# Kernel optimization log

Hardware: AMD Instinct MI355X
Metric: run time of the kernel (lower is better)

The kernel has to match this reference:

```python
import jax, jax.numpy as jnp
import numpy as np

B, S, D, H, L = 32, 1024, 512, 8, 4
DH = D // H
FF = D            # dim_feedforward == hidden_dim in the original ctor call
LOC_D, TD_D = 16, 8
TD_EMB = 3        # time_dist_embed_dim
POI = 21          # poi vocab
POI_EMB = 3
ADDR_IN = 1 + POI_EMB
FC = 32           # fc_hidden_dim
NEG = -1e9


def setup_inputs() -> dict:
    key = jax.random.key(0)
    ks = jax.random.split(key, 20)
    g = lambda i, shape, s=0.02: jax.random.normal(ks[i], shape, jnp.float32) * s
    return {
        "addr": jax.random.normal(ks[0], (B, 1), jnp.float32),
        "loc_dense_seq": jax.random.normal(ks[1], (B, S, LOC_D), jnp.float32),
        "time_dist_seq": jax.random.normal(ks[2], (B, S, TD_D), jnp.float32),
        "Wtd": g(3, (TD_D, TD_EMB)), "btd": jnp.zeros((TD_EMB,), jnp.float32),
        "Wemb": g(4, (LOC_D + TD_EMB, D)), "bemb": jnp.zeros((D,), jnp.float32),
        "Wqkv": g(5, (L, D, 3 * D)), "bqkv": jnp.zeros((L, 3 * D), jnp.float32),
        "Wo": g(6, (L, D, D)), "bo": jnp.zeros((L, D), jnp.float32),
        "ln1_g": jnp.ones((L, D), jnp.float32), "ln1_b": jnp.zeros((L, D), jnp.float32),
        "W1": g(7, (L, D, FF)), "b1": jnp.zeros((L, FF), jnp.float32),
        "W2": g(8, (L, FF, D)), "b2": jnp.zeros((L, D), jnp.float32),
        "ln2_g": jnp.ones((L, D), jnp.float32), "ln2_b": jnp.zeros((L, D), jnp.float32),
        "poi_emb": g(9, (POI, POI_EMB), 1.0),
        "Wa": g(10, (ADDR_IN, FC)), "ba": jnp.zeros((FC,), jnp.float32),
        "Wout": g(11, (D, FC)),
        "Wcomb": g(12, (FC, 1)),
        "addr_type": jax.random.randint(ks[13], (B, 1), 0, POI),
        "data_length": jax.random.randint(ks[14], (B,), 1, S + 1),
    }


def _ln(x, g, b, eps=1e-5):
    m = x.mean(-1, keepdims=True)
    v = ((x - m) ** 2).mean(-1, keepdims=True)
    return (x - m) / jnp.sqrt(v + eps) * g + b


def reference(addr, loc_dense_seq, time_dist_seq, Wtd, btd, Wemb, bemb, Wqkv,
              bqkv, Wo, bo, ln1_g, ln1_b, W1, b1, W2, b2, ln2_g, ln2_b,
              poi_emb, Wa, ba, Wout, Wcomb, addr_type, data_length):
    valid = jnp.arange(S)[None, :] < data_length[:, None]            # [B,S]
    td = time_dist_seq @ Wtd + btd                                   # [B,S,3]
    x = jnp.concatenate([loc_dense_seq, td], axis=-1) @ Wemb + bemb  # [B,S,D]
    scale = 1.0 / jnp.sqrt(jnp.float32(DH))
    for l in range(L):  # post-norm TransformerEncoderLayer (relu, eval/no-dropout)
        qkv = x @ Wqkv[l] + bqkv[l]
        q, k, v = jnp.split(qkv, 3, axis=-1)
        q = q.reshape(B, S, H, DH)
        k = k.reshape(B, S, H, DH)
        v = v.reshape(B, S, H, DH)
        scores = jnp.einsum('bqhd,bkhd->bhqk', q, k) * scale
        scores = jnp.where(valid[:, None, None, :], scores, NEG)     # mask padded keys
        attn = jax.nn.softmax(scores, axis=-1)
        ctx = jnp.einsum('bhqk,bkhd->bqhd', attn, v).reshape(B, S, D)
        x = _ln(x + ctx @ Wo[l] + bo[l], ln1_g[l], ln1_b[l])
        ff = jax.nn.relu(x @ W1[l] + b1[l]) @ W2[l] + b2[l]
        x = _ln(x + ff, ln2_g[l], ln2_b[l])
    # per-sample addr branch (vectorized over the original python loop)
    addr_inp = jnp.concatenate([addr, poi_emb[addr_type[:, 0]]], axis=-1)  # [B,4]
    a = addr_inp @ Wa + ba                                                 # [B,FC]
    o = (jnp.tanh(x @ Wout + a[:, None, :]) @ Wcomb)[..., 0]              # [B,S]
    logits = jnp.where(valid, o, NEG)
    logp = jax.nn.log_softmax(logits, axis=1)  # log_softmax over valid positions only
    return jnp.where(valid, logp, 0.0)
```

## Files before the change

kernel.cpp:

```cpp
#include <hip/hip_runtime.h>
#include <stdint.h>


typedef unsigned short u16;
typedef __attribute__((ext_vector_type(8))) short short8;
typedef __attribute__((ext_vector_type(4))) float f32x4;

constexpr int Bn = 32, Sn = 1024, Dn = 512, Ln = 4;
constexpr int BS = Bn * Sn;
constexpr size_t QKV_OFF = 16777216;

__device__ __forceinline__ float b2f(u16 u) {
    union { uint32_t i; float f; } v; v.i = ((uint32_t)u) << 16; return v.f;
}
__device__ __forceinline__ u16 f2b(float f) {
    union { float f; uint32_t i; } v; v.f = f;
    uint32_t r = v.i + 0x7fffu + ((v.i >> 16) & 1u);
    return (u16)(r >> 16);
}
__device__ __forceinline__ float getf(const void* p, size_t i, int F) {
    return F ? ((const float*)p)[i] : b2f(((const u16*)p)[i]);
}
__device__ __forceinline__ void cp16(void* lds, const void* g) {
    __builtin_amdgcn_global_load_lds(
        (__attribute__((address_space(1))) void*)(uintptr_t)g,
        (__attribute__((address_space(3))) void*)(uint32_t)(uintptr_t)lds,
        16, 0, 0);
}
__device__ __forceinline__ float asf(uint32_t u) {
    union { uint32_t i; float f; } v; v.i = u; return v.f;
}

__global__ __launch_bounds__(256)
void detect_kernel(const void* loc, int* flag)
{
    __shared__ int cnt;
    if (threadIdx.x == 0) cnt = 0;
    __syncthreads();
    const u16* p = (const u16*)loc;
    int c = 0;
    for (int i = threadIdx.x; i < 2048; i += 256) {
        const float v = b2f(p[i]);
        if (!(fabsf(v) <= 100.0f)) c++;
    }
    atomicAdd(&cnt, c);
    __syncthreads();
    if (threadIdx.x == 0) *flag = (cnt >= 64) ? 1 : 0;
}

__global__ __launch_bounds__(256)
void gemm_bt(const u16* __restrict__ A, const u16* __restrict__ Bt,
             const void* __restrict__ bias, int boff, u16* __restrict__ C,
             int N, int K, int relu, int mode, const int* __restrict__ flagp,
             const int* __restrict__ dlen)
{
    __shared__ __align__(16) u16 As[128 * 32];
    __shared__ __align__(16) u16 Bs[128 * 32];
    const int bn0 = blockIdx.x * 128, bm0 = blockIdx.y * 128;
    if ((bm0 & 1023) >= dlen[bm0 >> 10]) return;
    const int F = *flagp;
    const int tid = threadIdx.x;
    const int lane = tid & 63, w = tid >> 6;
    const int wm = w >> 1, wn = w & 1;
    const int quad = lane >> 4, l16 = lane & 15;

    const f32x4 vzero = {0.f, 0.f, 0.f, 0.f};
    f32x4 acc[4][4];
#pragma unroll
    for (int i = 0; i < 4; i++)
#pragma unroll
        for (int j = 0; j < 4; j++) acc[i][j] = vzero;

    const int i0 = tid, i1 = tid + 256;
    const u16* a0 = A + (size_t)(bm0 + (i0 >> 2)) * K + (i0 & 3) * 8;
    const u16* a1 = A + (size_t)(bm0 + (i1 >> 2)) * K + (i1 & 3) * 8;
    const u16* b0 = Bt + (size_t)(bn0 + (i0 >> 2)) * K + (i0 & 3) * 8;
    const u16* b1 = Bt + (size_t)(bn0 + (i1 >> 2)) * K + (i1 & 3) * 8;

    for (int k0 = 0; k0 < K; k0 += 32) {
        cp16(As + i0 * 8, a0 + k0);
        cp16(As + i1 * 8, a1 + k0);
        cp16(Bs + i0 * 8, b0 + k0);
        cp16(Bs + i1 * 8, b1 + k0);
        __syncthreads();
        short8 af[4], bfr[4];
#pragma unroll
        for (int t = 0; t < 4; t++)
            af[t] = *(const short8*)&As[(wm * 64 + t * 16 + l16) * 32 + quad * 8];
#pragma unroll
        for (int t = 0; t < 4; t++)
            bfr[t] = *(const short8*)&Bs[(wn * 64 + t * 16 + l16) * 32 + quad * 8];
#pragma unroll
        for (int tm = 0; tm < 4; tm++)
#pragma unroll
            for (int tn = 0; tn < 4; tn++)
                acc[tm][tn] = __builtin_amdgcn_mfma_f32_16x16x32_bf16(
                    af[tm], bfr[tn], acc[tm][tn], 0, 0, 0);
        __syncthreads();
    }
    const int bb = bm0 >> 10;
#pragma unroll
    for (int tm = 0; tm < 4; tm++)
#pragma unroll
        for (int tn = 0; tn < 4; tn++) {
            const int col = bn0 + wn * 64 + tn * 16 + l16;
            const float bv = getf(bias, (size_t)boff + col, F);
            if (mode == 0) {
#pragma unroll
                for (int r = 0; r < 4; r++) {
                    const int row = bm0 + wm * 64 + tm * 16 + quad * 4 + r;
                    float v = acc[tm][tn][r] + bv;
                    if (relu) v = fmaxf(v, 0.0f);
                    C[(size_t)row * N + col] = f2b(v);
                }
            } else {
                const int which = col >> 9;
                const int c = col & 511;
                const int hh = c >> 6, f = c & 63;
                u16* dst = C + (size_t)which * QKV_OFF
                           + (((size_t)(bb * 8 + hh)) << 16) + f;
#pragma unroll
                for (int r = 0; r < 4; r++) {
                    const int s = (bm0 & 1023) + wm * 64 + tm * 16 + quad * 4 + r;
                    dst[(size_t)s * 64] = f2b(acc[tm][tn][r] + bv);
                }
            }
        }
}

__global__ __launch_bounds__(256)
void attn_kernel(const u16* __restrict__ qp, const int* __restrict__ dlen,
                 u16* __restrict__ ctx)
{
    const int id = blockIdx.x;
    const int qt = 7 - (id >> 8);
    const int bh = id & 255;
    const int h = bh & 7, b = bh >> 3;
    const int len = dlen[b];
    if (qt * 128 >= len) return;
    const int tid = threadIdx.x, lane = tid & 63, w = tid >> 6;
    const int quad = lane >> 4, l16 = lane & 15;
    __shared__ __align__(16) u16 Vt[2][64 * 72];
    __shared__ __align__(16) u16 Pl[4][32 * 72];
    u16* Plw = Pl[w];
    const int sw = l16 & 3;
    const u16* qb = qp + ((size_t)bh << 16);
    const u16* kb = qb + QKV_OFF;
    const u16* vb = qb + 2 * QKV_OFF;
    const int q0 = qt * 128 + w * 32;
    constexpr float SC = 0.18033688011112043f;

    short8 qf[2][2];
#pragma unroll
    for (int sub = 0; sub < 2; sub++)
#pragma unroll
        for (int s = 0; s < 2; s++)
            qf[sub][s] = *(const short8*)(qb + (size_t)(q0 + sub * 16 + l16) * 64
                                          + quad * 8 + 32 * s);

    const int key2 = (tid & 31) * 2, f0 = (tid >> 5) * 8;
    const u16* vsrc = vb + f0;
    short8 v0 = *(const short8*)(vsrc + (size_t)key2 * 64);
    short8 v1 = *(const short8*)(vsrc + (size_t)(key2 + 1) * 64);

    short8 ones;
#pragma unroll
    for (int j = 0; j < 8; j++) ones[j] = (short)0x3F80;

    const f32x4 vzero = {0.f, 0.f, 0.f, 0.f};
    f32x4 O[2][4], lacc[2];
#pragma unroll
    for (int sub = 0; sub < 2; sub++) {
        lacc[sub] = vzero;
#pragma unroll
        for (int t = 0; t < 4; t++) O[sub][t] = vzero;
    }

    const int nkt = (len + 63) >> 6;
    int buf = 0;
    for (int kt = 0; kt < nkt; kt++) {
        const int k0 = kt * 64;
        u16* Vb = Vt[buf];
#pragma unroll
        for (int j = 0; j < 8; j++)
            *(uint32_t*)&Vb[(f0 + j) * 72 + key2] =
                (uint32_t)(u16)v0[j] | ((uint32_t)(u16)v1[j] << 16);
        __syncthreads();
        if (kt + 1 < nkt) {
            const u16* nv = vsrc + (size_t)(k0 + 64 + key2) * 64;
            v0 = *(const short8*)nv;
            v1 = *(const short8*)(nv + 64);
        }
        short8 kf[4][2];
#pragma unroll
        for (int tn = 0; tn < 4; tn++) {
            const u16* kp2 = kb + (size_t)(k0 + tn * 16 + l16) * 64 + quad * 8;
            kf[tn][0] = *(const short8*)kp2;
            kf[tn][1] = *(const short8*)(kp2 + 32);
        }
        const bool full = (k0 + 64 <= len);
#pragma unroll
        for (int sub = 0; sub < 2; sub++) {
            f32x4 sacc[4];
#pragma unroll
            for (int tn = 0; tn < 4; tn++) {
                f32x4 z = vzero;
                z = __builtin_amdgcn_mfma_f32_16x16x32_bf16(kf[tn][0], qf[sub][0], z, 0, 0, 0);
                sacc[tn] = __builtin_amdgcn_mfma_f32_16x16x32_bf16(kf[tn][1], qf[sub][1], z, 0, 0, 0);
            }
            const int prow = (sub * 16 + l16) * 72;
#pragma unroll
            for (int tn = 0; tn < 4; tn++) {
                float p[4];
                if (full) {
#pragma unroll
                    for (int r = 0; r < 4; r++) p[r] = exp2f(sacc[tn][r] * SC);
                } else {
                    const int kbnd = k0 + tn * 16 + quad * 4;
#pragma unroll
                    for (int r = 0; r < 4; r++)
                        p[r] = (kbnd + r < len) ? exp2f(sacc[tn][r] * SC) : 0.0f;
                }
                uint2 pk;
                pk.x = (__float_as_uint(p[0]) >> 16) | (__float_as_uint(p[1]) & 0xFFFF0000u);
                pk.y = (__float_as_uint(p[2]) >> 16) | (__float_as_uint(p[3]) & 0xFFFF0000u);
                *(uint2*)&Plw[prow + (((tn ^ sw) << 4) + quad * 4)] = pk;
            }
        }
        __builtin_amdgcn_wave_barrier();
#pragma unroll
        for (int s = 0; s < 2; s++) {
            const int tnr = ((quad >> 1) + 2 * s) ^ sw;
            short8 pf0 = *(const short8*)&Plw[(l16) * 72 + (tnr << 4) + (quad & 1) * 8];
            short8 pf1 = *(const short8*)&Plw[(16 + l16) * 72 + (tnr << 4) + (quad & 1) * 8];
            lacc[0] = __builtin_amdgcn_mfma_f32_16x16x32_bf16(pf0, ones, lacc[0], 0, 0, 0);
            lacc[1] = __builtin_amdgcn_mfma_f32_16x16x32_bf16(pf1, ones, lacc[1], 0, 0, 0);
#pragma unroll
            for (int t = 0; t < 4; t++) {
                short8 vf = *(const short8*)&Vb[(t * 16 + l16) * 72 + quad * 8 + 32 * s];
                O[0][t] = __builtin_amdgcn_mfma_f32_16x16x32_bf16(pf0, vf, O[0][t], 0, 0, 0);
                O[1][t] = __builtin_amdgcn_mfma_f32_16x16x32_bf16(pf1, vf, O[1][t], 0, 0, 0);
            }
        }
        __builtin_amdgcn_wave_barrier();
        buf ^= 1;
    }
#pragma unroll
    for (int sub = 0; sub < 2; sub++)
#pragma unroll
        for (int r = 0; r < 4; r++) {
            const float inv = 1.0f / lacc[sub][r];
            const int q = q0 + sub * 16 + quad * 4 + r;
#pragma unroll
            for (int t = 0; t < 4; t++)
                ctx[(size_t)(b * Sn + q) * Dn + h * 64 + t * 16 + l16] =
                    f2b(O[sub][t][r] * inv);
        }
}

__global__ __launch_bounds__(256)
void ln_res(u16* __restrict__ x, const u16* __restrict__ t,
            const void* __restrict__ g, const void* __restrict__ bta, int off,
            const int* __restrict__ flagp, const int* __restrict__ dlen)
{
    const int w = threadIdx.x >> 6, lane = threadIdx.x & 63;
    const size_t row = (size_t)blockIdx.x * 4 + w;
    if ((int)(row & 1023) >= dlen[row >> 10]) return;
    const int F = *flagp;
    u16* xp = x + row * Dn;
    const u16* tp = t + row * Dn;
    const int c0 = lane * 8;
    short8 xv = *(const short8*)(xp + c0);
    short8 tv = *(const short8*)(tp + c0);
    float v[8]; float s = 0.f;
#pragma unroll
    for (int i = 0; i < 8; i++) {
        v[i] = b2f((u16)xv[i]) + b2f((u16)tv[i]);
        s += v[i];
    }
#pragma unroll
    for (int o = 1; o < 64; o <<= 1) s += __shfl_xor(s, o, 64);
    const float mean = s * (1.0f / 512.0f);
    float q = 0.f;
#pragma unroll
    for (int i = 0; i < 8; i++) { const float d = v[i] - mean; q += d * d; }
#pragma unroll
    for (int o = 1; o < 64; o <<= 1) q += __shfl_xor(q, o, 64);
    const float inv = rsqrtf(q * (1.0f / 512.0f) + 1e-5f);
    short8 ov;
#pragma unroll
    for (int i = 0; i < 8; i++)
        ov[i] = (short)f2b((v[i] - mean) * inv * getf(g, off + c0 + i, F)
                           + getf(bta, off + c0 + i, F));
    *(short8*)(xp + c0) = ov;
}

__global__ __launch_bounds__(256)
void embed_kernel(const void* __restrict__ loc, const void* __restrict__ tds,
                  const void* __restrict__ Wtd, const void* __restrict__ btd,
                  const void* __restrict__ Wemb, const void* __restrict__ bemb,
                  u16* __restrict__ x, const int* __restrict__ flagp,
                  const int* __restrict__ dlen)
{
    const int token = blockIdx.x;
    if ((token & 1023) >= dlen[token >> 10]) return;
    const int F = *flagp;
    const int tid = threadIdx.x;
    __shared__ float inv[19];
    if (tid < 16) {
        inv[tid] = getf(loc, (size_t)token * 16 + tid, F);
    } else if (tid < 19) {
        const int e = tid - 16;
        float a = getf(btd, e, F);
        for (int j = 0; j < 8; j++)
            a += getf(tds, (size_t)token * 8 + j, F) * getf(Wtd, j * 3 + e, F);
        inv[tid] = a;
    }
    __syncthreads();
    for (int d = tid; d < Dn; d += 256) {
        float a = getf(bemb, d, F);
#pragma unroll
        for (int i = 0; i < 19; i++) a += inv[i] * getf(Wemb, (size_t)i * Dn + d, F);
        x[(size_t)token * Dn + d] = f2b(a);
    }
}

__global__ __launch_bounds__(256)
void transpose_w(const void* __restrict__ src, u16* __restrict__ dst,
                 int K, int N, const int* __restrict__ flagp)
{
    const int F = *flagp;
    __shared__ u16 tile[32][33];
    const size_t ls = (size_t)K * N;
    const size_t sb = (size_t)blockIdx.z * ls;
    u16* d = dst + blockIdx.z * ls;
    const int tx = threadIdx.x & 31, ty = threadIdx.x >> 5;
    const int n0 = blockIdx.x * 32, k0 = blockIdx.y * 32;
#pragma unroll
    for (int i = 0; i < 32; i += 8)
        tile[ty + i][tx] = f2b(getf(src, sb + (size_t)(k0 + ty + i) * N + n0 + tx, F));
    __syncthreads();
#pragma unroll
    for (int i = 0; i < 32; i += 8)
        d[(size_t)(n0 + ty + i) * K + k0 + tx] = tile[tx][ty + i];
}

__global__ __launch_bounds__(256)
void final_proj(const u16* __restrict__ x, const void* __restrict__ Wout,
                const void* __restrict__ Wcomb, const void* __restrict__ addr,
                const void* __restrict__ poi, const int* __restrict__ atype,
                const void* __restrict__ Wa, const void* __restrict__ ba,
                float* __restrict__ logits, const int* __restrict__ flagp,
                const int* __restrict__ dlen)
{
    const int t0 = blockIdx.x * 8;
    if ((t0 & 1023) >= dlen[t0 >> 10]) return;
    const int F = *flagp;
    __shared__ float xs[8][512];
    __shared__ __align__(8) u16 wlds[32 * 516];
    const int tid = threadIdx.x;
    for (int i = tid; i < 8 * 512; i += 256) {
        const int tk = i >> 9, d = i & 511;
        xs[tk][d] = b2f(x[(size_t)(t0 + tk) * Dn + d]);
    }
    for (int i = tid; i < 16384; i += 256) {
        const int k = i >> 5, j = i & 31;
        wlds[j * 516 + k] = F ? f2b(((const float*)Wout)[(size_t)k * 32 + j])
                              : ((const u16*)Wout)[(size_t)k * 32 + j];
    }
    __syncthreads();
    const int half = tid >> 5, j = tid & 31;
    const int token = t0 + half;
    const int b = token >> 10;
    if ((token & 1023) >= dlen[b]) return;
    const int ty = atype[b];
    float a = getf(ba, j, F) + getf(addr, b, F) * getf(Wa, j, F);
#pragma unroll
    for (int e = 0; e < 3; e++)
        a += getf(poi, ty * 3 + e, F) * getf(Wa, (1 + e) * 32 + j, F);
    float s = a;
    const u16* wj = wlds + j * 516;
    const float* xr = xs[half];
#pragma unroll 4
    for (int k = 0; k < 512; k += 4) {
        const uint2 wv = *(const uint2*)&wj[k];
        s += xr[k]     * asf(wv.x << 16);
        s += xr[k + 1] * asf(wv.x & 0xFFFF0000u);
        s += xr[k + 2] * asf(wv.y << 16);
        s += xr[k + 3] * asf(wv.y & 0xFFFF0000u);
    }
    float o = tanhf(s) * getf(Wcomb, j, F);
#pragma unroll
    for (int off = 1; off < 32; off <<= 1) o += __shfl_xor(o, off, 64);
    if (j == 0) logits[token] = o;
}

__global__ __launch_bounds__(256)
void lsm_kernel(const float* __restrict__ logits, const int* __restrict__ dlen,
                float* __restrict__ out)
{
    const int b = blockIdx.x, tid = threadIdx.x;
    const int len = dlen[b];
    const float* lp = logits + (size_t)b * Sn;
    __shared__ float wA[4], wB[4];
    float mx = -3e38f;
    for (int s = tid; s < Sn; s += 256) if (s < len) mx = fmaxf(mx, lp[s]);
#pragma unroll
    for (int o = 1; o < 64; o <<= 1) mx = fmaxf(mx, __shfl_xor(mx, o, 64));
    if ((tid & 63) == 0) wA[tid >> 6] = mx;
    __syncthreads();
    mx = fmaxf(fmaxf(wA[0], wA[1]), fmaxf(wA[2], wA[3]));
    float sm = 0.f;
    for (int s = tid; s < Sn; s += 256) if (s < len) sm += __expf(lp[s] - mx);
#pragma unroll
    for (int o = 1; o < 64; o <<= 1) sm += __shfl_xor(sm, o, 64);
    if ((tid & 63) == 0) wB[tid >> 6] = sm;
    __syncthreads();
    const float lse = mx + __logf(wB[0] + wB[1] + wB[2] + wB[3]);
    for (int s = tid; s < Sn; s += 256)
        out[(size_t)b * Sn + s] = (s < len) ? (lp[s] - lse) : 0.0f;
}

extern "C" void kernel_launch(void* const* d_in, const int* in_sizes, int n_in,
                              void* d_out, int out_size, void* d_ws, size_t ws_size,
                              hipStream_t stream) {
    const void* addr  = d_in[0];
    const void* loc   = d_in[1];
    const void* tds   = d_in[2];
    const void* Wtd   = d_in[3];
    const void* btd   = d_in[4];
    const void* Wemb  = d_in[5];
    const void* bemb  = d_in[6];
    const void* Wqkv  = d_in[7];
    const void* bqkv  = d_in[8];
    const void* Wo    = d_in[9];
    const void* bo    = d_in[10];
    const void* ln1g  = d_in[11];
    const void* ln1b  = d_in[12];
    const void* W1    = d_in[13];
    const void* b1    = d_in[14];
    const void* W2    = d_in[15];
    const void* b2    = d_in[16];
    const void* ln2g  = d_in[17];
    const void* ln2b  = d_in[18];
    const void* poi   = d_in[19];
    const void* Wa    = d_in[20];
    const void* ba    = d_in[21];
    const void* Wout  = d_in[22];
    const void* Wcomb = d_in[23];
    const int* atype  = (const int*)d_in[24];
    const int* dlen   = (const int*)d_in[25];

    char* base = (char*)d_ws;
    u16*   xb    = (u16*)(base);
    u16*   qkvp  = (u16*)(base + 33554432ull);
    u16*   ctxb  = (u16*)(base + 134217728ull);
    u16*   tb    = (u16*)(base + 167772160ull);
    u16*   wqkvT = (u16*)(base + 201326592ull);
    u16*   woT   = (u16*)(base + 207618048ull);
    u16*   w1T   = (u16*)(base + 209715200ull);
    u16*   w2T   = (u16*)(base + 211812352ull);
    float* logit = (float*)(base + 213909504ull);
    int*   flag  = (int*)  (base + 214040576ull);
    if (ws_size < 214040592ull) return;

    detect_kernel<<<1, 256, 0, stream>>>(loc, flag);

    transpose_w<<<dim3(48, 16, 4), 256, 0, stream>>>(Wqkv, wqkvT, 512, 1536, flag);
    transpose_w<<<dim3(16, 16, 4), 256, 0, stream>>>(Wo,   woT,   512, 512, flag);
    transpose_w<<<dim3(16, 16, 4), 256, 0, stream>>>(W1,   w1T,   512, 512, flag);
    transpose_w<<<dim3(16, 16, 4), 256, 0, stream>>>(W2,   w2T,   512, 512, flag);

    embed_kernel<<<BS, 256, 0, stream>>>(loc, tds, Wtd, btd, Wemb, bemb, xb, flag, dlen);

    for (int l = 0; l < Ln; l++) {
        gemm_bt<<<dim3(12, 256), 256, 0, stream>>>(
            xb, wqkvT + (size_t)l * 1536 * 512, bqkv, l * 1536, qkvp, 1536, 512, 0, 1, flag, dlen);
        attn_kernel<<<2048, 256, 0, stream>>>(qkvp, dlen, ctxb);
        gemm_bt<<<dim3(4, 256), 256, 0, stream>>>(
            ctxb, woT + (size_t)l * 512 * 512, bo, l * 512, tb, 512, 512, 0, 0, flag, dlen);
        ln_res<<<BS / 4, 256, 0, stream>>>(xb, tb, ln1g, ln1b, l * 512, flag, dlen);
        gemm_bt<<<dim3(4, 256), 256, 0, stream>>>(
            xb, w1T + (size_t)l * 512 * 512, b1, l * 512, ctxb, 512, 512, 1, 0, flag, dlen);
        gemm_bt<<<dim3(4, 256), 256, 0, stream>>>(
            ctxb, w2T + (size_t)l * 512 * 512, b2, l * 512, tb, 512, 512, 0, 0, flag, dlen);
        ln_res<<<BS / 4, 256, 0, stream>>>(xb, tb, ln2g, ln2b, l * 512, flag, dlen);
    }

    final_proj<<<BS / 8, 256, 0, stream>>>(xb, Wout, Wcomb, addr, poi, atype,
                                           Wa, ba, logit, flag, dlen);
    lsm_kernel<<<Bn, 256, 0, stream>>>(logit, dlen, (float*)d_out);
}
```

Before: 1.737 ms.

## Split attention key range across two blocks for long sequences and combine partials

For samples longer than 512 tokens, the attention grid is doubled. Each half processes a separate part of the key tiles and writes an unnormalized bf16 partial output plus fp32 row sums. A new combine kernel then adds the two partials and normalizes them. The aim is better load balance and more parallelism for long sequences, whose blocks otherwise form a long tail. The cost is an extra kernel launch, extra memory traffic, and bf16 rounding of the unnormalized partials. The split only turns on when the workspace is large enough.

```diff
diff --git a/kernel.cpp b/kernel.cpp
--- a/kernel.cpp
+++ b/kernel.cpp
@@ -130,14 +130,18 @@
 
 __global__ __launch_bounds__(256)
 void attn_kernel(const u16* __restrict__ qp, const int* __restrict__ dlen,
-                 u16* __restrict__ ctx)
+                 u16* __restrict__ ctx, u16* __restrict__ part,
+                 float* __restrict__ l0a, float* __restrict__ l1a, int split)
 {
     const int id = blockIdx.x;
-    const int qt = 7 - (id >> 8);
+    const int half = id >> 11;
+    const int qt = 7 - ((id >> 8) & 7);
     const int bh = id & 255;
     const int h = bh & 7, b = bh >> 3;
     const int len = dlen[b];
     if (qt * 128 >= len) return;
+    const int dosplit = split && (len > 512);
+    if (half && !dosplit) return;
     const int tid = threadIdx.x, lane = tid & 63, w = tid >> 6;
     const int quad = lane >> 4, l16 = lane & 15;
     __shared__ __align__(16) u16 Vt[2][64 * 72];
@@ -150,6 +154,10 @@
     const int q0 = qt * 128 + w * 32;
     constexpr float SC = 0.18033688011112043f;
 
+    const int nkt = (len + 63) >> 6;
+    int kt0 = 0, kt1 = nkt;
+    if (dosplit) { if (half) kt0 = 8; else kt1 = 8; }
+
     short8 qf[2][2];
 #pragma unroll
     for (int sub = 0; sub < 2; sub++)
@@ -160,8 +168,8 @@
 
     const int key2 = (tid & 31) * 2, f0 = (tid >> 5) * 8;
     const u16* vsrc = vb + f0;
-    short8 v0 = *(const short8*)(vsrc + (size_t)key2 * 64);
-    short8 v1 = *(const short8*)(vsrc + (size_t)(key2 + 1) * 64);
+    short8 v0 = *(const short8*)(vsrc + (size_t)(kt0 * 64 + key2) * 64);
+    short8 v1 = *(const short8*)(vsrc + (size_t)(kt0 * 64 + key2 + 1) * 64);
 
     short8 ones;
 #pragma unroll
@@ -176,9 +184,8 @@
         for (int t = 0; t < 4; t++) O[sub][t] = vzero;
     }
 
-    const int nkt = (len + 63) >> 6;
     int buf = 0;
-    for (int kt = 0; kt < nkt; kt++) {
+    for (int kt = kt0; kt < kt1; kt++) {
         const int k0 = kt * 64;
         u16* Vb = Vt[buf];
 #pragma unroll
@@ -186,7 +193,7 @@
             *(uint32_t*)&Vb[(f0 + j) * 72 + key2] =
                 (uint32_t)(u16)v0[j] | ((uint32_t)(u16)v1[j] << 16);
         __syncthreads();
-        if (kt + 1 < nkt) {
+        if (kt + 1 < kt1) {
             const u16* nv = vsrc + (size_t)(k0 + 64 + key2) * 64;
             v0 = *(const short8*)nv;
             v1 = *(const short8*)(nv + 64);
@@ -245,17 +252,65 @@
         __builtin_amdgcn_wave_barrier();
         buf ^= 1;
     }
-#pragma unroll
-    for (int sub = 0; sub < 2; sub++)
-#pragma unroll
-        for (int r = 0; r < 4; r++) {
-            const float inv = 1.0f / lacc[sub][r];
-            const int q = q0 + sub * 16 + quad * 4 + r;
-#pragma unroll
-            for (int t = 0; t < 4; t++)
-                ctx[(size_t)(b * Sn + q) * Dn + h * 64 + t * 16 + l16] =
-                    f2b(O[sub][t][r] * inv);
-        }
+
+    if (!dosplit) {
+#pragma unroll
+        for (int sub = 0; sub < 2; sub++)
+#pragma unroll
+            for (int r = 0; r < 4; r++) {
+                const float inv = 1.0f / lacc[sub][r];
+                const int q = q0 + sub * 16 + quad * 4 + r;
+#pragma unroll
+                for (int t = 0; t < 4; t++)
+                    ctx[(size_t)(b * Sn + q) * Dn + h * 64 + t * 16 + l16] =
+                        f2b(O[sub][t][r] * inv);
+            }
+    } else {
+        u16* dst = half ? part : ctx;
+        float* la = half ? l1a : l0a;
+        const int slot = (qt << 8) | bh;
+#pragma unroll
+        for (int sub = 0; sub < 2; sub++)
+#pragma unroll
+            for (int r = 0; r < 4; r++) {
+                const int q = q0 + sub * 16 + quad * 4 + r;
+#pragma unroll
+                for (int t = 0; t < 4; t++)
+                    dst[(size_t)(b * Sn + q) * Dn + h * 64 + t * 16 + l16] =
+                        f2b(O[sub][t][r]);
+                if (l16 == 0)
+                    la[slot * 128 + w * 32 + sub * 16 + quad * 4 + r] = lacc[sub][r];
+            }
+    }
+}
+
+__global__ __launch_bounds__(256)
+void attn_combine(u16* __restrict__ ctx, const u16* __restrict__ part,
+                  const float* __restrict__ l0a, const float* __restrict__ l1a,
+                  const int* __restrict__ dlen)
+{
+    const int id = blockIdx.x;
+    const int qt = id >> 8, bh = id & 255;
+    const int h = bh & 7, b = bh >> 3;
+    const int len = dlen[b];
+    if (len <= 512 || qt * 128 >= len) return;
+    const int tid = threadIdx.x;
+    const int ql = tid >> 1, fh = (tid & 1) * 32;
+    const int q = qt * 128 + ql;
+    const float inv = 1.0f / (l0a[id * 128 + ql] + l1a[id * 128 + ql]);
+    const size_t off = ((size_t)(b * Sn + q)) * Dn + h * 64 + fh;
+    u16* cp = ctx + off;
+    const u16* pp = part + off;
+#pragma unroll
+    for (int c = 0; c < 4; c++) {
+        short8 a = *(const short8*)(cp + c * 8);
+        short8 d = *(const short8*)(pp + c * 8);
+        short8 o;
+#pragma unroll
+        for (int j = 0; j < 8; j++)
+            o[j] = (short)f2b((b2f((u16)a[j]) + b2f((u16)d[j])) * inv);
+        *(short8*)(cp + c * 8) = o;
+    }
 }
 
 __global__ __launch_bounds__(256)
@@ -462,7 +517,10 @@
     u16*   w2T   = (u16*)(base + 211812352ull);
     float* logit = (float*)(base + 213909504ull);
     int*   flag  = (int*)  (base + 214040576ull);
+    float* l0a   = (float*)(base + 214040592ull);
+    float* l1a   = (float*)(base + 215089168ull);
     if (ws_size < 214040592ull) return;
+    const int split = (ws_size >= 216137744ull) ? 1 : 0;
 
     detect_kernel<<<1, 256, 0, stream>>>(loc, flag);
 
@@ -476,7 +534,9 @@
     for (int l = 0; l < Ln; l++) {
         gemm_bt<<<dim3(12, 256), 256, 0, stream>>>(
             xb, wqkvT + (size_t)l * 1536 * 512, bqkv, l * 1536, qkvp, 1536, 512, 0, 1, flag, dlen);
-        attn_kernel<<<2048, 256, 0, stream>>>(qkvp, dlen, ctxb);
+        attn_kernel<<<4096, 256, 0, stream>>>(qkvp, dlen, ctxb, tb, l0a, l1a, split);
+        if (split)
+            attn_combine<<<2048, 256, 0, stream>>>(ctxb, tb, l0a, l1a, dlen);
         gemm_bt<<<dim3(4, 256), 256, 0, stream>>>(
             ctxb, woT + (size_t)l * 512 * 512, bo, l * 512, tb, 512, 512, 0, 0, flag, dlen);
         ln_res<<<BS / 4, 256, 0, stream>>>(xb, tb, ln1g, ln1b, l * 512, flag, dlen);
```

New measurement: 1.852 ms. 1.07x slower.
